# Performance work log

Hardware: AMD Instinct MI355X
Metric: run time of the kernel (lower is better)

The kernel has to match this reference:

```python
import jax, jax.numpy as jnp
import numpy as np

H = 2048
B, L, S = 4, 4096, 10

def setup_inputs() -> dict:
    key = jax.random.key(0)
    k1, k2, k3, k4, k5, k6 = jax.random.split(key, 6)
    scale = 1.0 / np.sqrt(H)
    return {
        "h_english": jax.random.normal(k1, (B, L, H), dtype=jnp.float32),
        "h_lojban": jax.random.normal(k2, (B, S, H), dtype=jnp.float32),
        "w_q": jax.random.normal(k3, (H, H), dtype=jnp.float32) * scale,
        "w_k": jax.random.normal(k4, (H, H), dtype=jnp.float32) * scale,
        "w_v": jax.random.normal(k5, (H, H), dtype=jnp.float32) * scale,
        "w_o": jax.random.normal(k6, (H, H), dtype=jnp.float32) * scale,
        "alpha": jnp.float32(0.1),
    }

def reference(h_english, h_lojban, w_q, w_k, w_v, w_o, alpha):
    h = h_english.shape[-1]
    # torch Linear: y = x @ W^T
    q = jnp.einsum('blh,oh->blo', h_english, w_q)   # [B,L,H]
    k = jnp.einsum('bsh,oh->bso', h_lojban, w_k)    # [B,S,H]
    v = jnp.einsum('bsh,oh->bso', h_lojban, w_v)    # [B,S,H]
    scores = jnp.einsum('blh,bsh->bls', q, k) / jnp.sqrt(jnp.float32(h))  # [B,L,S]
    probs = jax.nn.softmax(scores, axis=-1)
    context = jnp.einsum('bls,bsh->blh', probs, v)  # [B,L,H]
    delta = jnp.einsum('blh,oh->blo', context, w_o)
    return h_english + alpha * delta
```

## Files before the change

kernel.cpp:

```cpp
#include <hip/hip_runtime.h>

#define SDIM 10
#define HDIM 2048
#define LDIM 4096
#define BDIM 4

#define KSCALE 0.02209708691207961f

__global__ __launch_bounds__(256) void kv_kernel(
    const float* __restrict__ h_l, const float* __restrict__ w_k,
    const float* __restrict__ w_v, float* __restrict__ k_out,
    float* __restrict__ v_out) {
  const int b = blockIdx.y;
  const int wave = threadIdx.x >> 6;
  const int lane = threadIdx.x & 63;
  const int opair = blockIdx.x * 4 + wave;
  const int o0 = opair * 2;

  const float4* hl4 = (const float4*)(h_l + (size_t)b * SDIM * HDIM);
  const float4* wk0 = (const float4*)(w_k + (size_t)o0 * HDIM);
  const float4* wk1 = (const float4*)(w_k + (size_t)(o0 + 1) * HDIM);
  const float4* wv0 = (const float4*)(w_v + (size_t)o0 * HDIM);
  const float4* wv1 = (const float4*)(w_v + (size_t)(o0 + 1) * HDIM);

  float ak0[SDIM], ak1[SDIM], av0[SDIM], av1[SDIM];
#pragma unroll
  for (int s = 0; s < SDIM; s++) { ak0[s] = ak1[s] = av0[s] = av1[s] = 0.f; }

#pragma unroll
  for (int j = 0; j < 8; j++) {
    const int idx = j * 64 + lane;
    const float4 a0 = wk0[idx], a1 = wk1[idx];
    const float4 c0 = wv0[idx], c1 = wv1[idx];
#pragma unroll
    for (int s = 0; s < SDIM; s++) {
      const float4 h = hl4[s * 512 + idx];
      ak0[s] += a0.x * h.x + a0.y * h.y + a0.z * h.z + a0.w * h.w;
      ak1[s] += a1.x * h.x + a1.y * h.y + a1.z * h.z + a1.w * h.w;
      av0[s] += c0.x * h.x + c0.y * h.y + c0.z * h.z + c0.w * h.w;
      av1[s] += c1.x * h.x + c1.y * h.y + c1.z * h.z + c1.w * h.w;
    }
  }
#pragma unroll
  for (int s = 0; s < SDIM; s++) {
#pragma unroll
    for (int d = 1; d < 64; d <<= 1) {
      ak0[s] += __shfl_xor(ak0[s], d);
      ak1[s] += __shfl_xor(ak1[s], d);
      av0[s] += __shfl_xor(av0[s], d);
      av1[s] += __shfl_xor(av1[s], d);
    }
  }
  if (lane == 0) {
#pragma unroll
    for (int s = 0; s < SDIM; s++) {
      const size_t base = ((size_t)b * SDIM + s) * HDIM + o0;
      k_out[base]     = ak0[s];
      k_out[base + 1] = ak1[s];
      v_out[base]     = av0[s];
      v_out[base + 1] = av1[s];
    }
  }
}

#define OSPLIT 16
__global__ __launch_bounds__(256) void kk_part_kernel(
    const float* __restrict__ k_in, const float* __restrict__ w_q,
    float* __restrict__ part) {
  const int b = blockIdx.z;
  const int oc = blockIdx.y >> 1;
  const int s0 = (blockIdx.y & 1) * 5;
  const int f4 = blockIdx.x * 256 + threadIdx.x;

  __shared__ float ksh[5 * 128];
  for (int idx = threadIdx.x; idx < 5 * 128; idx += 256) {
    const int s = idx >> 7, oo = idx & 127;
    ksh[idx] = k_in[((size_t)b * SDIM + s0 + s) * HDIM + oc * 128 + oo];
  }
  __syncthreads();

  float4 acc[5];
#pragma unroll
  for (int s = 0; s < 5; s++) acc[s] = make_float4(0.f, 0.f, 0.f, 0.f);

  const float4* wq4 = (const float4*)w_q;
  for (int oo = 0; oo < 128; oo++) {
    const float4 w = wq4[(size_t)(oc * 128 + oo) * 512 + f4];
#pragma unroll
    for (int s = 0; s < 5; s++) {
      const float kv = ksh[s * 128 + oo];
      acc[s].x += kv * w.x; acc[s].y += kv * w.y;
      acc[s].z += kv * w.z; acc[s].w += kv * w.w;
    }
  }
#pragma unroll
  for (int s = 0; s < 5; s++) {
    ((float4*)part)[(((size_t)oc * BDIM + b) * SDIM + s0 + s) * 512 + f4] = acc[s];
  }
}

__global__ __launch_bounds__(256) void kk_reduce_kernel(
    const float* __restrict__ part, float* __restrict__ kk_out) {
  const int t = blockIdx.x * 256 + threadIdx.x;
  const float4* p4 = (const float4*)part;
  float4 acc = make_float4(0.f, 0.f, 0.f, 0.f);
#pragma unroll
  for (int p = 0; p < OSPLIT; p++) {
    const float4 v = p4[(size_t)p * 20480 + t];
    acc.x += v.x; acc.y += v.y; acc.z += v.z; acc.w += v.w;
  }
  ((float4*)kk_out)[t] = acc;
}

__global__ __launch_bounds__(256) void vo_kernel(
    const float* __restrict__ v_in, const float* __restrict__ w_o,
    float* __restrict__ vo_out) {
  const int b = blockIdx.y;
  const int wave = threadIdx.x >> 6;
  const int lane = threadIdx.x & 63;
  const int opair = blockIdx.x * 4 + wave;
  const int o0 = opair * 2;

  const float4* vb4 = (const float4*)(v_in + (size_t)b * SDIM * HDIM);
  const float4* wo0 = (const float4*)(w_o + (size_t)o0 * HDIM);
  const float4* wo1 = (const float4*)(w_o + (size_t)(o0 + 1) * HDIM);

  float a0[SDIM], a1[SDIM];
#pragma unroll
  for (int s = 0; s < SDIM; s++) { a0[s] = a1[s] = 0.f; }

#pragma unroll
  for (int j = 0; j < 8; j++) {
    const int idx = j * 64 + lane;
    const float4 w0 = wo0[idx], w1 = wo1[idx];
#pragma unroll
    for (int s = 0; s < SDIM; s++) {
      const float4 h = vb4[s * 512 + idx];
      a0[s] += w0.x * h.x + w0.y * h.y + w0.z * h.z + w0.w * h.w;
      a1[s] += w1.x * h.x + w1.y * h.y + w1.z * h.z + w1.w * h.w;
    }
  }
#pragma unroll
  for (int s = 0; s < SDIM; s++) {
#pragma unroll
    for (int d = 1; d < 64; d <<= 1) {
      a0[s] += __shfl_xor(a0[s], d);
      a1[s] += __shfl_xor(a1[s], d);
    }
  }
  if (lane == 0) {
#pragma unroll
    for (int s = 0; s < SDIM; s++) {
      const size_t base = ((size_t)b * SDIM + s) * HDIM + o0;
      vo_out[base]     = a0[s];
      vo_out[base + 1] = a1[s];
    }
  }
}

__global__ __launch_bounds__(256) void attn_kernel(
    const float* __restrict__ h_e, const float* __restrict__ kk,
    const float* __restrict__ vo, const float* __restrict__ alpha_p,
    float* __restrict__ out) {
  const int b = blockIdx.y;
  const int wave = threadIdx.x >> 6;
  const int lane = threadIdx.x & 63;
  const int row0 = blockIdx.x * 8 + wave * 2;
  const float alpha = *alpha_p;
  const float4* kkb = (const float4*)(kk + (size_t)b * SDIM * HDIM);
  const float4* vob = (const float4*)(vo + (size_t)b * SDIM * HDIM);
  const size_t rowbase = ((size_t)b * LDIM + row0) * HDIM;

  float4 he[2][8];
#pragma unroll
  for (int r = 0; r < 2; r++) {
    const float4* src = (const float4*)(h_e + rowbase + (size_t)r * HDIM);
#pragma unroll
    for (int i = 0; i < 8; i++) he[r][i] = src[i * 64 + lane];
  }

  float acc[2][SDIM];
#pragma unroll
  for (int r = 0; r < 2; r++)
#pragma unroll
    for (int s = 0; s < SDIM; s++) acc[r][s] = 0.f;

#pragma unroll
  for (int i = 0; i < 8; i++) {
#pragma unroll
    for (int s = 0; s < SDIM; s++) {
      const float4 kv = kkb[s * 512 + i * 64 + lane];
#pragma unroll
      for (int r = 0; r < 2; r++)
        acc[r][s] += he[r][i].x * kv.x + he[r][i].y * kv.y +
                     he[r][i].z * kv.z + he[r][i].w * kv.w;
    }
  }

#pragma unroll
  for (int r = 0; r < 2; r++)
#pragma unroll
    for (int s = 0; s < SDIM; s++) {
      float v = acc[r][s];
      v += __shfl_xor(v, 1);
      v += __shfl_xor(v, 2);
      v += __shfl_xor(v, 4);
      v += __shfl_xor(v, 8);
      v += __shfl_xor(v, 16);
      v += __shfl_xor(v, 32);
      acc[r][s] = v * KSCALE;
    }

#pragma unroll
  for (int r = 0; r < 2; r++) {
    float m = acc[r][0];
#pragma unroll
    for (int s = 1; s < SDIM; s++) m = fmaxf(m, acc[r][s]);
    float sum = 0.f;
#pragma unroll
    for (int s = 0; s < SDIM; s++) {
      acc[r][s] = __expf(acc[r][s] - m);
      sum += acc[r][s];
    }
    const float inv = alpha / sum;
#pragma unroll
    for (int s = 0; s < SDIM; s++) acc[r][s] *= inv;
  }

#pragma unroll
  for (int i = 0; i < 8; i++) {
    float4 o4[2];
#pragma unroll
    for (int r = 0; r < 2; r++) o4[r] = he[r][i];
#pragma unroll
    for (int s = 0; s < SDIM; s++) {
      const float4 vv = vob[s * 512 + i * 64 + lane];
#pragma unroll
      for (int r = 0; r < 2; r++) {
        o4[r].x += acc[r][s] * vv.x;
        o4[r].y += acc[r][s] * vv.y;
        o4[r].z += acc[r][s] * vv.z;
        o4[r].w += acc[r][s] * vv.w;
      }
    }
#pragma unroll
    for (int r = 0; r < 2; r++)
      ((float4*)(out + rowbase + (size_t)r * HDIM))[i * 64 + lane] = o4[r];
  }
}

extern "C" void kernel_launch(void* const* d_in, const int* in_sizes, int n_in,
                              void* d_out, int out_size, void* d_ws, size_t ws_size,
                              hipStream_t stream) {
  const float* h_e   = (const float*)d_in[0];
  const float* h_l   = (const float*)d_in[1];
  const float* w_q   = (const float*)d_in[2];
  const float* w_k   = (const float*)d_in[3];
  const float* w_v   = (const float*)d_in[4];
  const float* w_o   = (const float*)d_in[5];
  const float* alpha = (const float*)d_in[6];
  float* out = (float*)d_out;

  float* ws      = (float*)d_ws;
  float* k_ws    = ws;
  float* v_ws    = ws + 81920;
  float* kk_ws   = ws + 163840;
  float* vo_ws   = ws + 245760;
  float* part_ws = ws + 327680;

  kv_kernel<<<dim3(256, BDIM), 256, 0, stream>>>(h_l, w_k, w_v, k_ws, v_ws);
  kk_part_kernel<<<dim3(2, 32, BDIM), 256, 0, stream>>>(k_ws, w_q, part_ws);
  vo_kernel<<<dim3(256, BDIM), 256, 0, stream>>>(v_ws, w_o, vo_ws);
  kk_reduce_kernel<<<80, 256, 0, stream>>>(part_ws, kk_ws);
  attn_kernel<<<dim3(512, BDIM), 256, 0, stream>>>(h_e, kk_ws, vo_ws, alpha, out);
}
```

Before: 412.1 us.

## Restructure weight-reading kernels to reuse weights across batches and stage K/V in LDS

kv_kernel and vo_kernel now assign each block a group of output rows, with waves covering all batches, so each weight row is read once for all four batches rather than once per batch. kk_part_kernel processes all ten S rows per block instead of splitting them in two, halving reads of w_q. attn_kernel uses 512-thread blocks and stages the kk and vo tables through shared memory in halves, accumulating directly into the h_english registers. The cost is more registers per thread, extra __syncthreads, and fewer blocks in the small kernels, which may reduce parallelism.

```diff
diff --git a/kernel.cpp b/kernel.cpp
--- a/kernel.cpp
+++ b/kernel.cpp
@@ -7,96 +7,101 @@
 
 #define KSCALE 0.02209708691207961f
 
-__global__ __launch_bounds__(256) void kv_kernel(
+__global__ __launch_bounds__(512) void kv_kernel(
     const float* __restrict__ h_l, const float* __restrict__ w_k,
     const float* __restrict__ w_v, float* __restrict__ k_out,
     float* __restrict__ v_out) {
-  const int b = blockIdx.y;
   const int wave = threadIdx.x >> 6;
   const int lane = threadIdx.x & 63;
-  const int opair = blockIdx.x * 4 + wave;
-  const int o0 = opair * 2;
+  const int b = wave & 3;
+  const int s0 = (wave >> 2) * 5;
+  const int og = blockIdx.x;
 
   const float4* hl4 = (const float4*)(h_l + (size_t)b * SDIM * HDIM);
-  const float4* wk0 = (const float4*)(w_k + (size_t)o0 * HDIM);
-  const float4* wk1 = (const float4*)(w_k + (size_t)(o0 + 1) * HDIM);
-  const float4* wv0 = (const float4*)(w_v + (size_t)o0 * HDIM);
-  const float4* wv1 = (const float4*)(w_v + (size_t)(o0 + 1) * HDIM);
-
-  float ak0[SDIM], ak1[SDIM], av0[SDIM], av1[SDIM];
-#pragma unroll
-  for (int s = 0; s < SDIM; s++) { ak0[s] = ak1[s] = av0[s] = av1[s] = 0.f; }
+  const float4* wk4[4];
+  const float4* wv4[4];
+#pragma unroll
+  for (int o = 0; o < 4; o++) {
+    wk4[o] = (const float4*)(w_k + (size_t)(og * 4 + o) * HDIM);
+    wv4[o] = (const float4*)(w_v + (size_t)(og * 4 + o) * HDIM);
+  }
+
+  float ak[4][5], av[4][5];
+#pragma unroll
+  for (int o = 0; o < 4; o++)
+#pragma unroll
+    for (int s = 0; s < 5; s++) { ak[o][s] = 0.f; av[o][s] = 0.f; }
 
 #pragma unroll
   for (int j = 0; j < 8; j++) {
     const int idx = j * 64 + lane;
-    const float4 a0 = wk0[idx], a1 = wk1[idx];
-    const float4 c0 = wv0[idx], c1 = wv1[idx];
-#pragma unroll
-    for (int s = 0; s < SDIM; s++) {
-      const float4 h = hl4[s * 512 + idx];
-      ak0[s] += a0.x * h.x + a0.y * h.y + a0.z * h.z + a0.w * h.w;
-      ak1[s] += a1.x * h.x + a1.y * h.y + a1.z * h.z + a1.w * h.w;
-      av0[s] += c0.x * h.x + c0.y * h.y + c0.z * h.z + c0.w * h.w;
-      av1[s] += c1.x * h.x + c1.y * h.y + c1.z * h.z + c1.w * h.w;
-    }
-  }
-#pragma unroll
-  for (int s = 0; s < SDIM; s++) {
-#pragma unroll
-    for (int d = 1; d < 64; d <<= 1) {
-      ak0[s] += __shfl_xor(ak0[s], d);
-      ak1[s] += __shfl_xor(ak1[s], d);
-      av0[s] += __shfl_xor(av0[s], d);
-      av1[s] += __shfl_xor(av1[s], d);
-    }
-  }
-  if (lane == 0) {
-#pragma unroll
-    for (int s = 0; s < SDIM; s++) {
-      const size_t base = ((size_t)b * SDIM + s) * HDIM + o0;
-      k_out[base]     = ak0[s];
-      k_out[base + 1] = ak1[s];
-      v_out[base]     = av0[s];
-      v_out[base + 1] = av1[s];
-    }
-  }
+    float4 wk[4], wv[4], hv[5];
+#pragma unroll
+    for (int o = 0; o < 4; o++) { wk[o] = wk4[o][idx]; wv[o] = wv4[o][idx]; }
+#pragma unroll
+    for (int s = 0; s < 5; s++) hv[s] = hl4[(size_t)(s0 + s) * 512 + idx];
+#pragma unroll
+    for (int o = 0; o < 4; o++)
+#pragma unroll
+      for (int s = 0; s < 5; s++) {
+        ak[o][s] += wk[o].x * hv[s].x + wk[o].y * hv[s].y +
+                    wk[o].z * hv[s].z + wk[o].w * hv[s].w;
+        av[o][s] += wv[o].x * hv[s].x + wv[o].y * hv[s].y +
+                    wv[o].z * hv[s].z + wv[o].w * hv[s].w;
+      }
+  }
+
+#pragma unroll
+  for (int o = 0; o < 4; o++)
+#pragma unroll
+    for (int s = 0; s < 5; s++) {
+      float vk = ak[o][s], vv = av[o][s];
+#pragma unroll
+      for (int d = 1; d < 64; d <<= 1) {
+        vk += __shfl_xor(vk, d);
+        vv += __shfl_xor(vv, d);
+      }
+      if (lane == 0) {
+        const size_t base = ((size_t)b * SDIM + s0 + s) * HDIM + og * 4 + o;
+        k_out[base] = vk;
+        v_out[base] = vv;
+      }
+    }
 }
 
 #define OSPLIT 16
 __global__ __launch_bounds__(256) void kk_part_kernel(
     const float* __restrict__ k_in, const float* __restrict__ w_q,
     float* __restrict__ part) {
-  const int b = blockIdx.z;
-  const int oc = blockIdx.y >> 1;
-  const int s0 = (blockIdx.y & 1) * 5;
-  const int f4 = blockIdx.x * 256 + threadIdx.x;
-
-  __shared__ float ksh[5 * 128];
-  for (int idx = threadIdx.x; idx < 5 * 128; idx += 256) {
+  const int ht = blockIdx.x;
+  const int oc = blockIdx.y;
+  const int b  = blockIdx.z;
+  const int f4 = ht * 256 + threadIdx.x;
+
+  __shared__ float ksh[SDIM * 128];
+  for (int idx = threadIdx.x; idx < SDIM * 128; idx += 256) {
     const int s = idx >> 7, oo = idx & 127;
-    ksh[idx] = k_in[((size_t)b * SDIM + s0 + s) * HDIM + oc * 128 + oo];
+    ksh[idx] = k_in[((size_t)b * SDIM + s) * HDIM + oc * 128 + oo];
   }
   __syncthreads();
 
-  float4 acc[5];
-#pragma unroll
-  for (int s = 0; s < 5; s++) acc[s] = make_float4(0.f, 0.f, 0.f, 0.f);
+  float4 acc[SDIM];
+#pragma unroll
+  for (int s = 0; s < SDIM; s++) acc[s] = make_float4(0.f, 0.f, 0.f, 0.f);
 
   const float4* wq4 = (const float4*)w_q;
   for (int oo = 0; oo < 128; oo++) {
     const float4 w = wq4[(size_t)(oc * 128 + oo) * 512 + f4];
 #pragma unroll
-    for (int s = 0; s < 5; s++) {
+    for (int s = 0; s < SDIM; s++) {
       const float kv = ksh[s * 128 + oo];
       acc[s].x += kv * w.x; acc[s].y += kv * w.y;
       acc[s].z += kv * w.z; acc[s].w += kv * w.w;
     }
   }
 #pragma unroll
-  for (int s = 0; s < 5; s++) {
-    ((float4*)part)[(((size_t)oc * BDIM + b) * SDIM + s0 + s) * 512 + f4] = acc[s];
-  }
+  for (int s = 0; s < SDIM; s++)
+    ((float4*)part)[(((size_t)oc * BDIM + b) * SDIM + s) * 512 + f4] = acc[s];
 }
 
 __global__ __launch_bounds__(256) void kk_reduce_kernel(
@@ -112,63 +117,67 @@
   ((float4*)kk_out)[t] = acc;
 }
 
-__global__ __launch_bounds__(256) void vo_kernel(
+__global__ __launch_bounds__(512) void vo_kernel(
     const float* __restrict__ v_in, const float* __restrict__ w_o,
     float* __restrict__ vo_out) {
+  const int wave = threadIdx.x >> 6;
+  const int lane = threadIdx.x & 63;
+  const int b = wave & 3;
+  const int s0 = (wave >> 2) * 5;
+  const int og = blockIdx.x;
+
+  const float4* vb4 = (const float4*)(v_in + (size_t)b * SDIM * HDIM);
+  const float4* wo4[8];
+#pragma unroll
+  for (int o = 0; o < 8; o++)
+    wo4[o] = (const float4*)(w_o + (size_t)(og * 8 + o) * HDIM);
+
+  float acc[8][5];
+#pragma unroll
+  for (int o = 0; o < 8; o++)
+#pragma unroll
+    for (int s = 0; s < 5; s++) acc[o][s] = 0.f;
+
+#pragma unroll
+  for (int j = 0; j < 8; j++) {
+    const int idx = j * 64 + lane;
+    float4 wo[8], hv[5];
+#pragma unroll
+    for (int o = 0; o < 8; o++) wo[o] = wo4[o][idx];
+#pragma unroll
+    for (int s = 0; s < 5; s++) hv[s] = vb4[(size_t)(s0 + s) * 512 + idx];
+#pragma unroll
+    for (int o = 0; o < 8; o++)
+#pragma unroll
+      for (int s = 0; s < 5; s++)
+        acc[o][s] += wo[o].x * hv[s].x + wo[o].y * hv[s].y +
+                     wo[o].z * hv[s].z + wo[o].w * hv[s].w;
+  }
+
+#pragma unroll
+  for (int o = 0; o < 8; o++)
+#pragma unroll
+    for (int s = 0; s < 5; s++) {
+      float v = acc[o][s];
+#pragma unroll
+      for (int d = 1; d < 64; d <<= 1) v += __shfl_xor(v, d);
+      if (lane == 0)
+        vo_out[((size_t)b * SDIM + s0 + s) * HDIM + og * 8 + o] = v;
+    }
+}
+
+__global__ __launch_bounds__(512, 4) void attn_kernel(
+    const float* __restrict__ h_e, const float* __restrict__ kk,
+    const float* __restrict__ vo, const float* __restrict__ alpha_p,
+    float* __restrict__ out) {
+  __shared__ float4 lds4[2560];
   const int b = blockIdx.y;
   const int wave = threadIdx.x >> 6;
   const int lane = threadIdx.x & 63;
-  const int opair = blockIdx.x * 4 + wave;
-  const int o0 = opair * 2;
-
-  const float4* vb4 = (const float4*)(v_in + (size_t)b * SDIM * HDIM);
-  const float4* wo0 = (const float4*)(w_o + (size_t)o0 * HDIM);
-  const float4* wo1 = (const float4*)(w_o + (size_t)(o0 + 1) * HDIM);
-
-  float a0[SDIM], a1[SDIM];
-#pragma unroll
-  for (int s = 0; s < SDIM; s++) { a0[s] = a1[s] = 0.f; }
-
-#pragma unroll
-  for (int j = 0; j < 8; j++) {
-    const int idx = j * 64 + lane;
-    const float4 w0 = wo0[idx], w1 = wo1[idx];
-#pragma unroll
-    for (int s = 0; s < SDIM; s++) {
-      const float4 h = vb4[s * 512 + idx];
-      a0[s] += w0.x * h.x + w0.y * h.y + w0.z * h.z + w0.w * h.w;
-      a1[s] += w1.x * h.x + w1.y * h.y + w1.z * h.z + w1.w * h.w;
-    }
-  }
-#pragma unroll
-  for (int s = 0; s < SDIM; s++) {
-#pragma unroll
-    for (int d = 1; d < 64; d <<= 1) {
-      a0[s] += __shfl_xor(a0[s], d);
-      a1[s] += __shfl_xor(a1[s], d);
-    }
-  }
-  if (lane == 0) {
-#pragma unroll
-    for (int s = 0; s < SDIM; s++) {
-      const size_t base = ((size_t)b * SDIM + s) * HDIM + o0;
-      vo_out[base]     = a0[s];
-      vo_out[base + 1] = a1[s];
-    }
-  }
-}
-
-__global__ __launch_bounds__(256) void attn_kernel(
-    const float* __restrict__ h_e, const float* __restrict__ kk,
-    const float* __restrict__ vo, const float* __restrict__ alpha_p,
-    float* __restrict__ out) {
-  const int b = blockIdx.y;
-  const int wave = threadIdx.x >> 6;
-  const int lane = threadIdx.x & 63;
-  const int row0 = blockIdx.x * 8 + wave * 2;
+  const int row0 = blockIdx.x * 16 + wave * 2;
   const float alpha = *alpha_p;
-  const float4* kkb = (const float4*)(kk + (size_t)b * SDIM * HDIM);
-  const float4* vob = (const float4*)(vo + (size_t)b * SDIM * HDIM);
+  const float4* kkb4 = (const float4*)(kk + (size_t)b * SDIM * HDIM);
+  const float4* vob4 = (const float4*)(vo + (size_t)b * SDIM * HDIM);
   const size_t rowbase = ((size_t)b * LDIM + row0) * HDIM;
 
   float4 he[2][8];
@@ -185,16 +194,20 @@
 #pragma unroll
     for (int s = 0; s < SDIM; s++) acc[r][s] = 0.f;
 
-#pragma unroll
-  for (int i = 0; i < 8; i++) {
-#pragma unroll
-    for (int s = 0; s < SDIM; s++) {
-      const float4 kv = kkb[s * 512 + i * 64 + lane];
-#pragma unroll
-      for (int r = 0; r < 2; r++)
-        acc[r][s] += he[r][i].x * kv.x + he[r][i].y * kv.y +
-                     he[r][i].z * kv.z + he[r][i].w * kv.w;
-    }
+  for (int half = 0; half < 2; half++) {
+    __syncthreads();
+    for (int t = threadIdx.x; t < 2560; t += 512) lds4[t] = kkb4[half * 2560 + t];
+    __syncthreads();
+#pragma unroll
+    for (int i = 0; i < 8; i++)
+#pragma unroll
+      for (int s = 0; s < 5; s++) {
+        const float4 kv = lds4[s * 512 + i * 64 + lane];
+#pragma unroll
+        for (int r = 0; r < 2; r++)
+          acc[r][half * 5 + s] += he[r][i].x * kv.x + he[r][i].y * kv.y +
+                                  he[r][i].z * kv.z + he[r][i].w * kv.w;
+      }
   }
 
 #pragma unroll
@@ -227,25 +240,31 @@
     for (int s = 0; s < SDIM; s++) acc[r][s] *= inv;
   }
 
-#pragma unroll
-  for (int i = 0; i < 8; i++) {
-    float4 o4[2];
-#pragma unroll
-    for (int r = 0; r < 2; r++) o4[r] = he[r][i];
-#pragma unroll
-    for (int s = 0; s < SDIM; s++) {
-      const float4 vv = vob[s * 512 + i * 64 + lane];
-#pragma unroll
-      for (int r = 0; r < 2; r++) {
-        o4[r].x += acc[r][s] * vv.x;
-        o4[r].y += acc[r][s] * vv.y;
-        o4[r].z += acc[r][s] * vv.z;
-        o4[r].w += acc[r][s] * vv.w;
-      }
-    }
-#pragma unroll
-    for (int r = 0; r < 2; r++)
-      ((float4*)(out + rowbase + (size_t)r * HDIM))[i * 64 + lane] = o4[r];
+  for (int half = 0; half < 2; half++) {
+    __syncthreads();
+    for (int t = threadIdx.x; t < 2560; t += 512) lds4[t] = vob4[half * 2560 + t];
+    __syncthreads();
+#pragma unroll
+    for (int i = 0; i < 8; i++)
+#pragma unroll
+      for (int s = 0; s < 5; s++) {
+        const float4 vv = lds4[s * 512 + i * 64 + lane];
+#pragma unroll
+        for (int r = 0; r < 2; r++) {
+          const float p = acc[r][half * 5 + s];
+          he[r][i].x += p * vv.x;
+          he[r][i].y += p * vv.y;
+          he[r][i].z += p * vv.z;
+          he[r][i].w += p * vv.w;
+        }
+      }
+  }
+
+#pragma unroll
+  for (int r = 0; r < 2; r++) {
+    float4* dst = (float4*)(out + rowbase + (size_t)r * HDIM);
+#pragma unroll
+    for (int i = 0; i < 8; i++) dst[i * 64 + lane] = he[r][i];
   }
 }
 
@@ -268,9 +287,9 @@
   float* vo_ws   = ws + 245760;
   float* part_ws = ws + 327680;
 
-  kv_kernel<<<dim3(256, BDIM), 256, 0, stream>>>(h_l, w_k, w_v, k_ws, v_ws);
-  kk_part_kernel<<<dim3(2, 32, BDIM), 256, 0, stream>>>(k_ws, w_q, part_ws);
-  vo_kernel<<<dim3(256, BDIM), 256, 0, stream>>>(v_ws, w_o, vo_ws);
+  kv_kernel<<<512, 512, 0, stream>>>(h_l, w_k, w_v, k_ws, v_ws);
+  kk_part_kernel<<<dim3(2, OSPLIT, BDIM), 256, 0, stream>>>(k_ws, w_q, part_ws);
   kk_reduce_kernel<<<80, 256, 0, stream>>>(part_ws, kk_ws);
-  attn_kernel<<<dim3(512, BDIM), 256, 0, stream>>>(h_e, kk_ws, vo_ws, alpha, out);
-}
+  vo_kernel<<<256, 512, 0, stream>>>(v_ws, w_o, vo_ws);
+  attn_kernel<<<dim3(256, BDIM), 512, 0, stream>>>(h_e, kk_ws, vo_ws, alpha, out);
+}
```

After: 971.5 us. 136% more time.
